# Kernel tuning notes

Measured on AMD Instinct MI355X. Metric: run time of the kernel, lower is better.

The kernel has to match this reference:

```python
import jax, jax.numpy as jnp
import numpy as np

N = 50000   # nodes
E = 800000  # edges (avg degree 16)
F = 96      # num_features
H = 96      # hidden_channels
G = 64      # graphs in batch
ALPHA = 0.5


def setup_inputs() -> dict:
    key = jax.random.key(0)
    ks = jax.random.split(key, 32)
    inp = {
        "x": jax.random.normal(ks[0], (N, F), jnp.float32),
        "edge_index": jax.random.randint(ks[1], (2, E), 0, N, dtype=jnp.int32),
        "batch": jnp.sort(jax.random.randint(ks[2], (N,), 0, G, dtype=jnp.int32)),
    }
    i = 3
    dims = [(F, H), (H, H), (H, H)]
    for l, (din, dout) in enumerate(dims, start=1):
        for tag in ("Wself", "Wsd", "Wds"):
            inp[f"{tag}{l}"] = jax.random.normal(ks[i], (din, dout), jnp.float32) * 0.05; i += 1
        for tag in ("bself", "bsd", "bds"):
            inp[f"{tag}{l}"] = jax.random.normal(ks[i], (dout,), jnp.float32) * 0.05; i += 1
    inp["lin1_w"] = jax.random.normal(ks[i], (H, 5), jnp.float32) * 0.05; i += 1
    inp["lin1_b"] = jax.random.normal(ks[i], (5,), jnp.float32) * 0.05; i += 1
    inp["lin2_w"] = jax.random.normal(ks[i], (5, 1), jnp.float32) * 0.05; i += 1
    inp["lin2_b"] = jax.random.normal(ks[i], (1,), jnp.float32) * 0.05
    return inp


def _agg_mean(x, idx_from, idx_to, n):
    # scatter-mean of x[idx_from] onto idx_to (PyG SAGEConv mean aggregation;
    # nodes with no incoming edges get 0)
    s = jax.ops.segment_sum(x[idx_from], idx_to, num_segments=n)
    c = jax.ops.segment_sum(jnp.ones((idx_to.shape[0],), x.dtype), idx_to, num_segments=n)
    return s / jnp.maximum(c, 1.0)[:, None]


def _dir_sage(x, src, dst, Wself, bself, Wsd, bsd, Wds, bds):
    n = x.shape[0]
    out_self = x @ Wself + bself
    # source_to_target: aggregate x[src] at dst; target_to_source: aggregate x[dst] at src
    out_sd = _agg_mean(x, src, dst, n) @ Wsd + bsd
    out_ds = _agg_mean(x, dst, src, n) @ Wds + bds
    return out_self + (1.0 - ALPHA) * out_sd + ALPHA * out_ds


def reference(x, edge_index, batch,
              Wself1, bself1, Wsd1, bsd1, Wds1, bds1,
              Wself2, bself2, Wsd2, bsd2, Wds2, bds2,
              Wself3, bself3, Wsd3, bsd3, Wds3, bds3,
              lin1_w, lin1_b, lin2_w, lin2_b):
    src, dst = edge_index[0], edge_index[1]
    h = jax.nn.relu(_dir_sage(x, src, dst, Wself1, bself1, Wsd1, bsd1, Wds1, bds1))
    h = jax.nn.relu(_dir_sage(h, src, dst, Wself2, bself2, Wsd2, bsd2, Wds2, bds2))
    h = jax.nn.relu(_dir_sage(h, src, dst, Wself3, bself3, Wsd3, bsd3, Wds3, bds3))
    g = jax.ops.segment_max(h, batch, num_segments=G)  # global_max_pool -> [G, H]
    g = jax.nn.relu(g @ lin1_w + lin1_b)
    return g @ lin2_w + lin2_b  # [G, 1]
```

## Files before the change

kernel.cpp:

```cpp
#include <hip/hip_runtime.h>
#include <hip/hip_bf16.h>

#define HF 96
#define GG 64
#define DEG 64
#define CAPB 4608
#define CPAD 100
#define APAD 296

typedef __attribute__((ext_vector_type(8))) short bf16x8;
typedef __attribute__((ext_vector_type(4))) float f32x4;
typedef unsigned int uint;

__device__ __forceinline__ unsigned short f2bf(float f) {
    unsigned u = __float_as_uint(f);
    unsigned r = (u + 0x7FFFu + ((u >> 16) & 1u)) >> 16;
    return (unsigned short)r;
}
__device__ __forceinline__ float bf2f(unsigned short h) {
    return __uint_as_float(((unsigned)h) << 16);
}

__device__ __forceinline__ uint4 pack_hilo4(float f0, float f1, float f2, float f3) {
    unsigned short h0 = f2bf(f0), h1 = f2bf(f1), h2 = f2bf(f2), h3 = f2bf(f3);
    unsigned short l0 = f2bf(f0 - bf2f(h0)), l1 = f2bf(f1 - bf2f(h1));
    unsigned short l2 = f2bf(f2 - bf2f(h2)), l3 = f2bf(f3 - bf2f(h3));
    uint4 o;
    o.x = (uint)h0 | ((uint)h1 << 16);
    o.y = (uint)h2 | ((uint)h3 << 16);
    o.z = (uint)l0 | ((uint)l1 << 16);
    o.w = (uint)l2 | ((uint)l3 << 16);
    return o;
}

__device__ __forceinline__ void acc_hilo4(float4& a, uint4 w) {
    a.x += __uint_as_float(w.x << 16) + __uint_as_float(w.z << 16);
    a.y += __uint_as_float(w.x & 0xFFFF0000u) + __uint_as_float(w.z & 0xFFFF0000u);
    a.z += __uint_as_float(w.y << 16) + __uint_as_float(w.w << 16);
    a.w += __uint_as_float(w.y & 0xFFFF0000u) + __uint_as_float(w.w & 0xFFFF0000u);
}

__global__ __launch_bounds__(256) void build_phase1(
        const float* __restrict__ x, const int* __restrict__ ei,
        unsigned short* __restrict__ hbuf,
        uint* __restrict__ pcnt, uint* __restrict__ pq, unsigned* __restrict__ g,
        const float* Ws1, const float* Wsd1, const float* Wds1,
        const float* bs1, const float* bsd1, const float* bds1,
        const float* Ws2, const float* Wsd2, const float* Wds2,
        const float* bs2, const float* bsd2, const float* bds2,
        const float* Ws3, const float* Wsd3, const float* Wds3,
        const float* bs3, const float* bsd3, const float* bds3,
        unsigned short* __restrict__ Whi3, unsigned short* __restrict__ Wlo3,
        float* __restrict__ bc3, int N, int E, int NB, int CE) {
    if (blockIdx.x < 256) {
        __shared__ int hist[512];
        __shared__ int lbase[512];
        for (int i = threadIdx.x; i < NB; i += 256) hist[i] = 0;
        __syncthreads();
        const int e0 = blockIdx.x * CE;
        int e1 = e0 + CE; if (e1 > E) e1 = E;
        for (int e = e0 + threadIdx.x; e < e1; e += 256) {
            int s = ei[e], d = ei[E + e];
            atomicAdd(&hist[d >> 8], 1);
            atomicAdd(&hist[(N + s) >> 8], 1);
        }
        __syncthreads();
        for (int b = threadIdx.x; b < NB; b += 256) {
            int h = hist[b];
            lbase[b] = h ? (int)atomicAdd(&pcnt[b], (uint)h) : 0;
        }
        __syncthreads();
        for (int e = e0 + threadIdx.x; e < e1; e += 256) {
            int s = ei[e], d = ei[E + e];
            int b0 = d >> 8;
            int p0 = atomicAdd(&lbase[b0], 1);
            if (p0 < CAPB) pq[(long long)b0 * CAPB + p0] = ((uint)(d & 255) << 16) | (uint)s;
            int k1 = N + s;
            int b1 = k1 >> 8;
            int p1 = atomicAdd(&lbase[b1], 1);
            if (p1 < CAPB) pq[(long long)b1 * CAPB + p1] = ((uint)(k1 & 255) << 16) | (uint)d;
        }
        return;
    }
    int t = (blockIdx.x - 256) * 256 + threadIdx.x;
    const int R0 = N * 24;
    if (t < R0) {
        int n = t / 24, q = t % 24;
        float4 v = *(const float4*)(x + (long long)n * HF + q * 4);
        *(uint4*)(hbuf + ((long long)n * 192 + q * 8)) = pack_hilo4(v.x, v.y, v.z, v.w);
        return;
    }
    t -= R0;
    if (t < GG * HF) { g[t] = 0u; return; }
    t -= GG * HF;
    const int PER = HF * 288 + HF;
    if (t >= 3 * PER) return;
    int l = t / PER;
    int idx = t % PER;
    const float* Wself = (l == 0) ? Ws1 : (l == 1) ? Ws2 : Ws3;
    const float* Wsd   = (l == 0) ? Wsd1 : (l == 1) ? Wsd2 : Wsd3;
    const float* Wds   = (l == 0) ? Wds1 : (l == 1) ? Wds2 : Wds3;
    const float* bself = (l == 0) ? bs1 : (l == 1) ? bs2 : bs3;
    const float* bsd   = (l == 0) ? bsd1 : (l == 1) ? bsd2 : bsd3;
    const float* bds   = (l == 0) ? bds1 : (l == 1) ? bds2 : bds3;
    unsigned short* Whi = Whi3 + (long long)l * HF * 288;
    unsigned short* Wlo = Wlo3 + (long long)l * HF * 288;
    float* bc = bc3 + l * HF;
    if (idx < HF * 288) {
        int j = idx / 288;
        int kk = idx % 288;
        int m = kk / HF, k = kk % HF;
        const float* W = (m == 0) ? Wself : (m == 1) ? Wsd : Wds;
        float w = W[k * HF + j];
        unsigned short hi = f2bf(w);
        Whi[idx] = hi;
        Wlo[idx] = f2bf(w - bf2f(hi));
    } else {
        int j = idx - HF * 288;
        bc[j] = bself[j] + 0.5f * (bsd[j] + bds[j]);
    }
}

__global__ __launch_bounds__(256) void build_phase2(
        const uint* __restrict__ pcnt, const uint* __restrict__ pq,
        int* __restrict__ cnt, int* __restrict__ nbr, int N) {
    int b = blockIdx.x;
    __shared__ int lcnt[256];
    lcnt[threadIdx.x] = 0;
    __syncthreads();
    int tot = (int)pcnt[b]; if (tot > CAPB) tot = CAPB;
    const uint* q = pq + (long long)b * CAPB;
    for (int i = threadIdx.x; i < tot; i += 256) {
        uint p = q[i];
        int lk = (int)(p >> 16);
        int v = (int)(p & 0xFFFFu);
        int slot = atomicAdd(&lcnt[lk], 1);
        long long k = ((long long)b << 8) + lk;
        if (slot < DEG) nbr[(k << 6) + slot] = v;
    }
    __syncthreads();
    long long k = ((long long)b << 8) + threadIdx.x;
    if (k < 2LL * N) cnt[k] = lcnt[threadIdx.x];
}

__global__ __launch_bounds__(256) void gather_kernel(
        const unsigned short* __restrict__ hbuf, unsigned short* __restrict__ abuf,
        const int* __restrict__ cnt, const int* __restrict__ nbr, int N) {
    int t = blockIdx.x * blockDim.x + threadIdx.x;
    int P = t / 24;
    if (P >= 2 * N) return;
    int q = t % 24;
    int dir = (P >= N) ? 1 : 0;
    int n = P - dir * N;

    int degt = cnt[P];
    int deg = (degt > DEG) ? DEG : degt;
    const int* nb = nbr + ((long long)P << 6);

    const unsigned short* xq = hbuf + q * 8;
    float4 a0 = make_float4(0.f, 0.f, 0.f, 0.f);
    float4 a1 = a0, a2 = a0, a3 = a0;
    int i = 0;
    for (; i + 4 <= deg; i += 4) {
        int i0 = nb[i + 0], i1 = nb[i + 1], i2 = nb[i + 2], i3 = nb[i + 3];
        uint4 w0 = *(const uint4*)(xq + (long long)i0 * 192);
        uint4 w1 = *(const uint4*)(xq + (long long)i1 * 192);
        uint4 w2 = *(const uint4*)(xq + (long long)i2 * 192);
        uint4 w3 = *(const uint4*)(xq + (long long)i3 * 192);
        acc_hilo4(a0, w0);
        acc_hilo4(a1, w1);
        acc_hilo4(a2, w2);
        acc_hilo4(a3, w3);
    }
    for (; i < deg; i++) {
        uint4 w0 = *(const uint4*)(xq + (long long)nb[i] * 192);
        acc_hilo4(a0, w0);
    }
    float4 acc;
    acc.x = (a0.x + a1.x) + (a2.x + a3.x);
    acc.y = (a0.y + a1.y) + (a2.y + a3.y);
    acc.z = (a0.z + a1.z) + (a2.z + a3.z);
    acc.w = (a0.w + a1.w) + (a2.w + a3.w);
    float inv = 0.5f / fmaxf((float)degt, 1.0f);
    acc.x *= inv; acc.y *= inv; acc.z *= inv; acc.w *= inv;
    *(uint4*)(abuf + ((long long)n * 384 + (dir * 24 + q) * 8)) =
        pack_hilo4(acc.x, acc.y, acc.z, acc.w);
}

__global__ __launch_bounds__(256, 2) void sage_mfma(
        const unsigned short* __restrict__ hbuf, const unsigned short* __restrict__ abuf,
        unsigned short* __restrict__ hout,
        const unsigned short* __restrict__ Whi_g, const unsigned short* __restrict__ Wlo_g,
        const float* __restrict__ bc, const int* __restrict__ batch,
        unsigned* __restrict__ gmax, int mode, int N) {
    __shared__ __align__(16) unsigned short AH[64 * APAD];
    __shared__ __align__(16) unsigned short AL[64 * APAD];
    float* C = (float*)AH;

    const int tx = threadIdx.x;
    const int lane = tx & 63;
    const int wid = tx >> 6;
    const int wr = (wid >> 1) * 32;
    const int wc = (wid & 1) * 48;
    const int m = lane & 15;
    const int quad = lane >> 4;
    const int row0 = blockIdx.x * 64;

    {
        const int arow = tx >> 2;
        const int aj = tx & 3;
        int garc = row0 + arow; if (garc > N - 1) garc = N - 1;
        const unsigned short* hrow = hbuf + (long long)garc * 192;
        const unsigned short* grow = abuf + (long long)garc * 384;
#pragma unroll
        for (int cc = 0; cc < 18; cc++) {
            int c = cc * 4 + aj;
            const unsigned short* src = (c < 24) ? (hrow + c * 8) : (grow + (c - 24) * 8);
            uint4 v = *(const uint4*)src;
            *(uint2*)&AH[arow * APAD + c * 4] = make_uint2(v.x, v.y);
            *(uint2*)&AL[arow * APAD + c * 4] = make_uint2(v.z, v.w);
        }
    }
    __syncthreads();

    f32x4 acc[2][3];
#pragma unroll
    for (int rt = 0; rt < 2; rt++)
#pragma unroll
        for (int ct = 0; ct < 3; ct++) acc[rt][ct] = (f32x4){0.f, 0.f, 0.f, 0.f};

    int abase[2];
#pragma unroll
    for (int rt = 0; rt < 2; rt++) abase[rt] = (wr + rt * 16 + m) * APAD + quad * 8;
    long long wbase[3];
#pragma unroll
    for (int ct = 0; ct < 3; ct++) wbase[ct] = (long long)(wc + ct * 16 + m) * 288 + quad * 8;

#pragma unroll 3
    for (int kt = 0; kt < 9; kt++) {
        const int kg = kt * 32;
        bf16x8 ah[2], al[2], bh[3], bl[3];
#pragma unroll
        for (int rt = 0; rt < 2; rt++) {
            ah[rt] = *(const bf16x8*)&AH[abase[rt] + kg];
            al[rt] = *(const bf16x8*)&AL[abase[rt] + kg];
        }
#pragma unroll
        for (int ct = 0; ct < 3; ct++) {
            bh[ct] = *(const bf16x8*)(Whi_g + wbase[ct] + kg);
            bl[ct] = *(const bf16x8*)(Wlo_g + wbase[ct] + kg);
        }
#pragma unroll
        for (int rt = 0; rt < 2; rt++)
#pragma unroll
            for (int ct = 0; ct < 3; ct++) {
                acc[rt][ct] = __builtin_amdgcn_mfma_f32_16x16x32_bf16(ah[rt], bh[ct], acc[rt][ct], 0, 0, 0);
                acc[rt][ct] = __builtin_amdgcn_mfma_f32_16x16x32_bf16(ah[rt], bl[ct], acc[rt][ct], 0, 0, 0);
                acc[rt][ct] = __builtin_amdgcn_mfma_f32_16x16x32_bf16(al[rt], bh[ct], acc[rt][ct], 0, 0, 0);
            }
    }
    __syncthreads();

#pragma unroll
    for (int ct = 0; ct < 3; ct++) {
        int col = wc + ct * 16 + m;
        float bcv = bc[col];
#pragma unroll
        for (int rt = 0; rt < 2; rt++) {
#pragma unroll
            for (int reg = 0; reg < 4; reg++) {
                int rl = wr + rt * 16 + quad * 4 + reg;
                C[rl * CPAD + col] = fmaxf(acc[rt][ct][reg] + bcv, 0.f);
            }
        }
    }
    __syncthreads();

    if (mode == 0) {
        int rl = tx >> 2;
        int aj = tx & 3;
        int r = row0 + rl;
        if (r < N) {
            unsigned short* Orow = hout + (long long)r * 192;
#pragma unroll
            for (int k = 0; k < 6; k++) {
                int c = aj * 6 + k;
                const float* src = &C[rl * CPAD + c * 4];
                *(uint4*)(Orow + c * 8) = pack_hilo4(src[0], src[1], src[2], src[3]);
            }
        }
    } else {
        if (tx < HF) {
            int j = tx;
            int rmax = N - row0; if (rmax > 64) rmax = 64;
            float cur = 0.0f;
            int curb = -1;
            for (int r = 0; r < rmax; r++) {
                int bt = batch[row0 + r];
                float v = C[r * CPAD + j];
                if (bt != curb) {
                    if (curb >= 0) atomicMax(&gmax[curb * HF + j], __float_as_uint(cur));
                    curb = bt;
                    cur = v;
                } else {
                    cur = fmaxf(cur, v);
                }
            }
            if (curb >= 0) atomicMax(&gmax[curb * HF + j], __float_as_uint(cur));
        }
    }
}

__global__ void mlp_kernel(const unsigned* __restrict__ g, const float* __restrict__ lin1_w,
                           const float* __restrict__ lin1_b, const float* __restrict__ lin2_w,
                           const float* __restrict__ lin2_b, float* __restrict__ out) {
    int gi = threadIdx.x;
    if (gi >= GG) return;
    float h5[5];
#pragma unroll
    for (int hh = 0; hh < 5; hh++) {
        float acc = lin1_b[hh];
#pragma unroll 8
        for (int k = 0; k < HF; k++)
            acc = fmaf(__uint_as_float(g[gi * HF + k]), lin1_w[k * 5 + hh], acc);
        h5[hh] = fmaxf(acc, 0.0f);
    }
    float o = lin2_b[0];
#pragma unroll
    for (int hh = 0; hh < 5; hh++) o = fmaf(h5[hh], lin2_w[hh * 1 + 0], o);
    out[gi] = o;
}

extern "C" void kernel_launch(void* const* d_in, const int* in_sizes, int n_in,
                              void* d_out, int out_size, void* d_ws, size_t ws_size,
                              hipStream_t stream) {
    const float* x     = (const float*)d_in[0];
    const int*   ei    = (const int*)d_in[1];
    const int*   batch = (const int*)d_in[2];
    const float* W[3][3];
    const float* B[3][3];
    for (int l = 0; l < 3; l++) {
        for (int t = 0; t < 3; t++) W[l][t] = (const float*)d_in[3 + l * 6 + t];
        for (int t = 0; t < 3; t++) B[l][t] = (const float*)d_in[3 + l * 6 + 3 + t];
    }
    const float* lin1_w = (const float*)d_in[21];
    const float* lin1_b = (const float*)d_in[22];
    const float* lin2_w = (const float*)d_in[23];
    const float* lin2_b = (const float*)d_in[24];

    const int N = in_sizes[0] / HF;
    const int E = in_sizes[1] / 2;
    const int NB = (2 * N + 255) / 256;
    const int CE = (E + 255) / 256;

    unsigned short* hbuf = (unsigned short*)d_ws;
    unsigned short* abuf = hbuf + (long long)N * 192;
    int* cnt = (int*)(abuf + (long long)N * 384);
    int* nbr = cnt + 2LL * N;
    uint* pcnt = (uint*)(nbr + 2LL * N * DEG);
    uint* pq = pcnt + NB;
    float* bc3 = (float*)(pq + (long long)NB * CAPB);
    uintptr_t p = (uintptr_t)(bc3 + 3 * HF);
    p = (p + 15) & ~(uintptr_t)15;
    unsigned short* Whi3 = (unsigned short*)p;
    unsigned short* Wlo3 = Whi3 + 3 * HF * 288;
    uintptr_t p2 = (uintptr_t)(Wlo3 + 3 * HF * 288);
    p2 = (p2 + 15) & ~(uintptr_t)15;
    unsigned* g = (unsigned*)p2;

    hipMemsetAsync(pcnt, 0, (size_t)NB * sizeof(uint), stream);

    const long long lin_threads = (long long)N * 24 + GG * HF + 3LL * (HF * 288 + HF);
    const int lin_blocks = (int)((lin_threads + 255) / 256);
    build_phase1<<<256 + lin_blocks, 256, 0, stream>>>(
        x, ei, hbuf, pcnt, pq, g,
        W[0][0], W[0][1], W[0][2], B[0][0], B[0][1], B[0][2],
        W[1][0], W[1][1], W[1][2], B[1][0], B[1][1], B[1][2],
        W[2][0], W[2][1], W[2][2], B[2][0], B[2][1], B[2][2],
        Whi3, Wlo3, bc3, N, E, NB, CE);
    build_phase2<<<NB, 256, 0, stream>>>(pcnt, pq, cnt, nbr, N);

    const long long gather_threads = (long long)2 * N * 24;
    const int gather_blocks = (int)((gather_threads + 255) / 256);
    const int gemm_blocks = (N + 63) / 64;

    for (int l = 0; l < 3; l++) {
        gather_kernel<<<gather_blocks, 256, 0, stream>>>(hbuf, abuf, cnt, nbr, N);
        sage_mfma<<<gemm_blocks, 256, 0, stream>>>(
            hbuf, abuf, hbuf,
            Whi3 + (long long)l * HF * 288, Wlo3 + (long long)l * HF * 288,
            bc3 + l * HF, batch, g, (l < 2) ? 0 : 1, N);
    }

    mlp_kernel<<<1, 64, 0, stream>>>(g, lin1_w, lin1_b, lin2_w, lin2_b, (float*)d_out);
}
```

Before: 475.9 us.

## Stage weights in LDS and double GEMM row tile to 128 with K-loop streaming

The sage_mfma GEMM now handles 128 rows per block instead of 64. It streams the A tile (hi/lo bf16 split) and the weight tile through LDS one 32-wide K slice at a time, where before it loaded all of K for A up front and read weights straight from global memory. Weights are reused across more rows, and LDS per block shrinks to about 50KB. In exchange there are two barriers per K step with no double buffering, fewer blocks (about 391 on a large GPU), and more accumulator registers.

```diff
diff --git a/kernel.cpp b/kernel.cpp
--- a/kernel.cpp
+++ b/kernel.cpp
@@ -6,7 +6,7 @@
 #define DEG 64
 #define CAPB 4608
 #define CPAD 100
-#define APAD 296
+#define LPAD 40
 
 typedef __attribute__((ext_vector_type(8))) short bf16x8;
 typedef __attribute__((ext_vector_type(4))) float f32x4;
@@ -187,86 +187,95 @@
         pack_hilo4(acc.x, acc.y, acc.z, acc.w);
 }
 
-__global__ __launch_bounds__(256, 2) void sage_mfma(
+__global__ __launch_bounds__(256) void sage_mfma(
         const unsigned short* __restrict__ hbuf, const unsigned short* __restrict__ abuf,
         unsigned short* __restrict__ hout,
         const unsigned short* __restrict__ Whi_g, const unsigned short* __restrict__ Wlo_g,
         const float* __restrict__ bc, const int* __restrict__ batch,
         unsigned* __restrict__ gmax, int mode, int N) {
-    __shared__ __align__(16) unsigned short AH[64 * APAD];
-    __shared__ __align__(16) unsigned short AL[64 * APAD];
-    float* C = (float*)AH;
+    __shared__ __align__(16) unsigned char POOL[51200];
+    unsigned short* Ahi = (unsigned short*)POOL;
+    unsigned short* Alo = Ahi + 128 * LPAD;
+    unsigned short* Whs = Alo + 128 * LPAD;
+    unsigned short* Wls = Whs + 96 * LPAD;
+    float* C = (float*)POOL;
 
     const int tx = threadIdx.x;
     const int lane = tx & 63;
     const int wid = tx >> 6;
-    const int wr = (wid >> 1) * 32;
+    const int wr = (wid >> 1) * 64;
     const int wc = (wid & 1) * 48;
     const int m = lane & 15;
     const int quad = lane >> 4;
-    const int row0 = blockIdx.x * 64;
-
-    {
-        const int arow = tx >> 2;
-        const int aj = tx & 3;
-        int garc = row0 + arow; if (garc > N - 1) garc = N - 1;
-        const unsigned short* hrow = hbuf + (long long)garc * 192;
-        const unsigned short* grow = abuf + (long long)garc * 384;
-#pragma unroll
-        for (int cc = 0; cc < 18; cc++) {
-            int c = cc * 4 + aj;
-            const unsigned short* src = (c < 24) ? (hrow + c * 8) : (grow + (c - 24) * 8);
-            uint4 v = *(const uint4*)src;
-            *(uint2*)&AH[arow * APAD + c * 4] = make_uint2(v.x, v.y);
-            *(uint2*)&AL[arow * APAD + c * 4] = make_uint2(v.z, v.w);
-        }
-    }
-    __syncthreads();
-
-    f32x4 acc[2][3];
-#pragma unroll
-    for (int rt = 0; rt < 2; rt++)
+    const int row0 = blockIdx.x * 128;
+
+    const int arow = tx >> 2;
+    const int aj = tx & 3;
+    int garc0 = row0 + arow;      if (garc0 > N - 1) garc0 = N - 1;
+    int garc1 = row0 + arow + 64; if (garc1 > N - 1) garc1 = N - 1;
+
+    f32x4 acc[4][3];
+#pragma unroll
+    for (int rt = 0; rt < 4; rt++)
 #pragma unroll
         for (int ct = 0; ct < 3; ct++) acc[rt][ct] = (f32x4){0.f, 0.f, 0.f, 0.f};
 
-    int abase[2];
-#pragma unroll
-    for (int rt = 0; rt < 2; rt++) abase[rt] = (wr + rt * 16 + m) * APAD + quad * 8;
-    long long wbase[3];
-#pragma unroll
-    for (int ct = 0; ct < 3; ct++) wbase[ct] = (long long)(wc + ct * 16 + m) * 288 + quad * 8;
-
-#pragma unroll 3
     for (int kt = 0; kt < 9; kt++) {
-        const int kg = kt * 32;
-        bf16x8 ah[2], al[2], bh[3], bl[3];
-#pragma unroll
-        for (int rt = 0; rt < 2; rt++) {
-            ah[rt] = *(const bf16x8*)&AH[abase[rt] + kg];
-            al[rt] = *(const bf16x8*)&AL[abase[rt] + kg];
+        const int kglob = kt * 32;
+
+#pragma unroll
+        for (int h = 0; h < 2; h++) {
+            int garc = h ? garc1 : garc0;
+            int lrow = arow + h * 64;
+            const unsigned short* src;
+            if (kt < 3)      src = hbuf + (long long)garc * 192 + (kt * 8 + aj * 2) * 8;
+            else if (kt < 6) src = abuf + (long long)garc * 384 + ((kt - 3) * 8 + aj * 2) * 8;
+            else             src = abuf + (long long)garc * 384 + 192 + ((kt - 6) * 8 + aj * 2) * 8;
+            uint4 v0 = *(const uint4*)src;
+            uint4 v1 = *(const uint4*)(src + 8);
+            *(uint2*)&Ahi[lrow * LPAD + aj * 8 + 0] = make_uint2(v0.x, v0.y);
+            *(uint2*)&Alo[lrow * LPAD + aj * 8 + 0] = make_uint2(v0.z, v0.w);
+            *(uint2*)&Ahi[lrow * LPAD + aj * 8 + 4] = make_uint2(v1.x, v1.y);
+            *(uint2*)&Alo[lrow * LPAD + aj * 8 + 4] = make_uint2(v1.z, v1.w);
+        }
+        for (int s = tx; s < 384; s += 256) {
+            int n = s >> 2, q2 = s & 3;
+            long long go = (long long)n * 288 + kglob + q2 * 8;
+            *(bf16x8*)&Whs[n * LPAD + q2 * 8] = *(const bf16x8*)(Whi_g + go);
+            *(bf16x8*)&Wls[n * LPAD + q2 * 8] = *(const bf16x8*)(Wlo_g + go);
+        }
+        __syncthreads();
+
+        bf16x8 ah[4], al[4], bh[3], bl[3];
+#pragma unroll
+        for (int rt = 0; rt < 4; rt++) {
+            int r = (wr + rt * 16 + m) * LPAD + quad * 8;
+            ah[rt] = *(const bf16x8*)&Ahi[r];
+            al[rt] = *(const bf16x8*)&Alo[r];
         }
 #pragma unroll
         for (int ct = 0; ct < 3; ct++) {
-            bh[ct] = *(const bf16x8*)(Whi_g + wbase[ct] + kg);
-            bl[ct] = *(const bf16x8*)(Wlo_g + wbase[ct] + kg);
-        }
-#pragma unroll
-        for (int rt = 0; rt < 2; rt++)
+            int r = (wc + ct * 16 + m) * LPAD + quad * 8;
+            bh[ct] = *(const bf16x8*)&Whs[r];
+            bl[ct] = *(const bf16x8*)&Wls[r];
+        }
+#pragma unroll
+        for (int rt = 0; rt < 4; rt++)
 #pragma unroll
             for (int ct = 0; ct < 3; ct++) {
                 acc[rt][ct] = __builtin_amdgcn_mfma_f32_16x16x32_bf16(ah[rt], bh[ct], acc[rt][ct], 0, 0, 0);
                 acc[rt][ct] = __builtin_amdgcn_mfma_f32_16x16x32_bf16(ah[rt], bl[ct], acc[rt][ct], 0, 0, 0);
                 acc[rt][ct] = __builtin_amdgcn_mfma_f32_16x16x32_bf16(al[rt], bh[ct], acc[rt][ct], 0, 0, 0);
             }
-    }
-    __syncthreads();
+        __syncthreads();
+    }
 
 #pragma unroll
     for (int ct = 0; ct < 3; ct++) {
         int col = wc + ct * 16 + m;
         float bcv = bc[col];
 #pragma unroll
-        for (int rt = 0; rt < 2; rt++) {
+        for (int rt = 0; rt < 4; rt++) {
 #pragma unroll
             for (int reg = 0; reg < 4; reg++) {
                 int rl = wr + rt * 16 + quad * 4 + reg;
@@ -277,14 +286,14 @@
     __syncthreads();
 
     if (mode == 0) {
-        int rl = tx >> 2;
-        int aj = tx & 3;
+        int rl = tx >> 1;
+        int half = tx & 1;
         int r = row0 + rl;
         if (r < N) {
             unsigned short* Orow = hout + (long long)r * 192;
 #pragma unroll
-            for (int k = 0; k < 6; k++) {
-                int c = aj * 6 + k;
+            for (int k = 0; k < 12; k++) {
+                int c = half * 12 + k;
                 const float* src = &C[rl * CPAD + c * 4];
                 *(uint4*)(Orow + c * 8) = pack_hilo4(src[0], src[1], src[2], src[3]);
             }
@@ -292,7 +301,7 @@
     } else {
         if (tx < HF) {
             int j = tx;
-            int rmax = N - row0; if (rmax > 64) rmax = 64;
+            int rmax = N - row0; if (rmax > 128) rmax = 128;
             float cur = 0.0f;
             int curb = -1;
             for (int r = 0; r < rmax; r++) {
@@ -382,7 +391,7 @@
 
     const long long gather_threads = (long long)2 * N * 24;
     const int gather_blocks = (int)((gather_threads + 255) / 256);
-    const int gemm_blocks = (N + 63) / 64;
+    const int gemm_blocks = (N + 127) / 128;
 
     for (int l = 0; l < 3; l++) {
         gather_kernel<<<gather_blocks, 256, 0, stream>>>(hbuf, abuf, cnt, nbr, N);
```

Result: no change. 474.2 us (-0.3%).
